# Optimization experiments

Hardware: AMD Instinct MI355X
Metric: run time of the kernel (lower is better)

## Reference

```python
import jax, jax.numpy as jnp
import numpy as np

N_POINTS = 1_500_000
N_SUPERPOINTS = 50_000
FEAT_DIM = 32
HIDDEN_DIM = 64
EMBED_DIM = 128


def setup_inputs() -> dict:
    key = jax.random.key(0)
    k1, k2, k3, k4, k5, k6 = jax.random.split(key, 6)
    return {
        "full_features": jax.random.normal(k1, (N_POINTS, FEAT_DIM), dtype=jnp.float32),
        "super_indices": jax.random.randint(k2, (N_POINTS,), 0, N_SUPERPOINTS, dtype=jnp.int64)
        if jax.config.jax_enable_x64 else jax.random.randint(k2, (N_POINTS,), 0, N_SUPERPOINTS, dtype=jnp.int32),
        "W1": jax.random.normal(k3, (FEAT_DIM, HIDDEN_DIM), dtype=jnp.float32) * 0.1,
        "b1": jax.random.normal(k4, (HIDDEN_DIM,), dtype=jnp.float32) * 0.01,
        "W2": jax.random.normal(k5, (HIDDEN_DIM, EMBED_DIM), dtype=jnp.float32) * 0.1,
        "b2": jax.random.normal(k6, (EMBED_DIM,), dtype=jnp.float32) * 0.01,
    }


def reference(full_features, super_indices, W1, b1, W2, b2):
    # Fused gather -> 2-layer MLP -> per-superpoint max reduction.
    # Equivalent to SuperPointNet.gen_token_embed, vectorized over all
    # superpoints instead of a Python loop with boolean-mask gathers.
    h = jax.nn.relu(full_features @ W1 + b1)          # [N, HIDDEN]
    h = jax.nn.relu(h @ W2 + b2)                      # [N, EMBED]
    sp_features = jax.ops.segment_max(
        h, super_indices, num_segments=N_SUPERPOINTS, indices_are_sorted=False
    )                                                  # [NS, EMBED]
    # Guard empty superpoints (segment_max yields -inf); original loop
    # assumes every superpoint id is present.
    sp_features = jnp.where(jnp.isfinite(sp_features), sp_features, 0.0)
    return sp_features
```

## Files before the change

kernel.cpp:

```cpp
#include <hip/hip_runtime.h>
#include <hip/hip_bf16.h>


#define NPTS 1500000
#define NSEG 50000
#define CAP  120

typedef __attribute__((ext_vector_type(8))) short short8;
typedef __attribute__((ext_vector_type(4))) float floatx4;
typedef __attribute__((ext_vector_type(2))) float floatx2;

__device__ __forceinline__ unsigned short f2bf(float f) {
    unsigned int x = __float_as_uint(f);
    x += 0x7FFFu + ((x >> 16) & 1u);
    return (unsigned short)(x >> 16);
}
__device__ __forceinline__ float bf2f(unsigned short b) {
    return __uint_as_float(((unsigned int)b) << 16);
}
__device__ __forceinline__ unsigned cvt_pk_bf16(float lo, float hi) {
    unsigned r;
    asm("v_cvt_pk_bf16_f32 %0, %1, %2" : "=v"(r) : "v"(lo), "v"(hi));
    return r;
}

__device__ __forceinline__ short8 load_x(const void* Xv, int pid, int quad, int isbf)
{
    if (isbf) {
        return *(const short8*)((const unsigned short*)Xv + (size_t)pid * 32 + quad * 8);
    } else {
        const float* xf = (const float*)Xv + (size_t)pid * 32 + quad * 8;
        const floatx4 f0 = *(const floatx4*)xf;
        const floatx4 f1 = *(const floatx4*)(xf + 4);
        union { short8 s; unsigned u[4]; } a;
        a.u[0] = cvt_pk_bf16(f0[0], f0[1]);
        a.u[1] = cvt_pk_bf16(f0[2], f0[3]);
        a.u[2] = cvt_pk_bf16(f1[0], f1[1]);
        a.u[3] = cvt_pk_bf16(f1[2], f1[3]);
        return a.s;
    }
}

__device__ __forceinline__ int probe_idx64(const unsigned* idxw, unsigned* scnt)
{
    if (threadIdx.x == 0) *scnt = 0u;
    __syncthreads();
    int nz = 0;
    #pragma unroll
    for (int j = 0; j < 2; ++j)
        nz += (idxw[(threadIdx.x * 2 + j) * 2 + 1] != 0u) ? 1 : 0;
    atomicAdd(scnt, (unsigned)nz);
    __syncthreads();
    return (*scnt < 256u) ? 1 : 0;
}

__device__ __forceinline__ int probe_isbf(const unsigned* Xw, unsigned* scnt)
{
    if (threadIdx.x == 0) *scnt = 0u;
    __syncthreads();
    int c = 0;
    #pragma unroll
    for (int j = 0; j < 4; ++j) {
        unsigned u  = Xw[threadIdx.x * 4 + j];
        unsigned he = (u >> 23) & 0xFFu, le = (u >> 7) & 0xFFu;
        c += (he >= 100u && he <= 140u && le >= 100u && le <= 140u) ? 1 : 0;
    }
    atomicAdd(scnt, (unsigned)c);
    __syncthreads();
    return (*scnt >= 512u) ? 1 : 0;
}

__global__ __launch_bounds__(256)
void build_slots(const unsigned* __restrict__ idxw,
                 const unsigned* __restrict__ Xw,
                 unsigned* __restrict__ cnt,
                 int* __restrict__ slots,
                 unsigned* __restrict__ flags)
{
    __shared__ unsigned sc;
    const int idx64 = probe_idx64(idxw, &sc);

    if (blockIdx.x == 0) {
        __syncthreads();
        const int isbf = probe_isbf(Xw, &sc);
        if (threadIdx.x == 0) flags[0] = (unsigned)isbf;
    }

    const int S  = gridDim.x * 256;
    const int i0 = blockIdx.x * 256 + threadIdx.x;
    const int i1 = i0 + S, i2 = i1 + S;

    unsigned s0 = 0xFFFFFFFFu, s1 = 0xFFFFFFFFu, s2 = 0xFFFFFFFFu;
    if (i0 < NPTS) s0 = idx64 ? idxw[2 * (size_t)i0] : idxw[i0];
    if (i1 < NPTS) s1 = idx64 ? idxw[2 * (size_t)i1] : idxw[i1];
    if (i2 < NPTS) s2 = idx64 ? idxw[2 * (size_t)i2] : idxw[i2];

    unsigned p0 = 0, p1 = 0, p2 = 0;
    if (s0 < NSEG) p0 = atomicAdd(&cnt[s0], 1u);
    if (s1 < NSEG) p1 = atomicAdd(&cnt[s1], 1u);
    if (s2 < NSEG) p2 = atomicAdd(&cnt[s2], 1u);

    if (s0 < NSEG && p0 < CAP) slots[(size_t)s0 * CAP + p0] = i0;
    if (s1 < NSEG && p1 < CAP) slots[(size_t)s1 * CAP + p1] = i1;
    if (s2 < NSEG && p2 < CAP) slots[(size_t)s2 * CAP + p2] = i2;
}

template<int DT>
__global__ __launch_bounds__(256)
void seg_mlp_max(const void* __restrict__ Xv,
                 const void* __restrict__ W1v, const void* __restrict__ B1v,
                 const void* __restrict__ W2v, const void* __restrict__ B2v,
                 const unsigned* __restrict__ cnt,
                 const int* __restrict__ slots,
                 const unsigned* __restrict__ flags,
                 void* __restrict__ outv)
{
    if (flags[0] != (unsigned)DT) return;

    __shared__ __align__(16) float outs[4][128];

    const int tid = threadIdx.x, wave = tid >> 6, lane = tid & 63;
    const int quad = lane >> 4, l16 = lane & 15;

    short8 w1f[4];
    #pragma unroll
    for (int t = 0; t < 4; ++t)
        #pragma unroll
        for (int j = 0; j < 8; ++j) {
            const int e = (quad * 8 + j) * 64 + t * 16 + l16;
            w1f[t][j] = DT ? (short)((const unsigned short*)W1v)[e]
                           : (short)f2bf(((const float*)W1v)[e]);
        }

    short8 w2f[2][8];
    #pragma unroll
    for (int kt = 0; kt < 2; ++kt)
        #pragma unroll
        for (int t = 0; t < 8; ++t)
            #pragma unroll
            for (int j = 0; j < 8; ++j) {
                const int k = kt * 32 + (j >> 2) * 16 + quad * 4 + (j & 3);
                const int e = k * 128 + t * 16 + l16;
                w2f[kt][t][j] = DT ? (short)((const unsigned short*)W2v)[e]
                                   : (short)f2bf(((const float*)W2v)[e]);
            }

    float b1v[16];
    #pragma unroll
    for (int t = 0; t < 4; ++t)
        #pragma unroll
        for (int r = 0; r < 4; ++r) {
            const int n = t * 16 + quad * 4 + r;
            b1v[t * 4 + r] = DT ? bf2f(((const unsigned short*)B1v)[n])
                                : ((const float*)B1v)[n];
        }
    float b2v[8];
    #pragma unroll
    for (int t = 0; t < 8; ++t)
        b2v[t] = DT ? bf2f(((const unsigned short*)B2v)[t * 16 + l16])
                    : ((const float*)B2v)[t * 16 + l16];

    float* fs = outs[wave];
    const int gw = blockIdx.x * 4 + wave, nw = gridDim.x * 4;

    for (int seg = gw; seg < NSEG; seg += nw) {
        const int c = min((int)cnt[seg], CAP);

        float vmax[8];
        #pragma unroll
        for (int t = 0; t < 8; ++t) vmax[t] = 0.f;

        if (c > 0) {
            const int nt = (c + 15) >> 4, last = c - 1;
            const size_t base = (size_t)seg * CAP;

            short8 abuf[2];
            abuf[0] = load_x(Xv, slots[base + min(l16, last)], quad, DT);
            if (nt > 1)
                abuf[1] = load_x(Xv, slots[base + min(16 + l16, last)], quad, DT);

            for (int ti = 0; ti < nt; ++ti) {
                const short8 acur = abuf[ti & 1];
                if (ti + 2 < nt)
                    abuf[ti & 1] = load_x(
                        Xv, slots[base + min((ti + 2) * 16 + l16, last)], quad, DT);

                floatx4 c1[4];
                #pragma unroll
                for (int t = 0; t < 4; ++t) {
                    floatx4 z = {0.f, 0.f, 0.f, 0.f};
                    c1[t] = __builtin_amdgcn_mfma_f32_16x16x32_bf16(w1f[t], acur, z, 0, 0, 0);
                }

                union { short8 s; unsigned u[4]; } af0, af1;
                #pragma unroll
                for (int t = 0; t < 4; ++t) {
                    const float h0 = fmaxf(c1[t][0] + b1v[t * 4 + 0], 0.f);
                    const float h1 = fmaxf(c1[t][1] + b1v[t * 4 + 1], 0.f);
                    const float h2 = fmaxf(c1[t][2] + b1v[t * 4 + 2], 0.f);
                    const float h3 = fmaxf(c1[t][3] + b1v[t * 4 + 3], 0.f);
                    const unsigned lo = cvt_pk_bf16(h0, h1);
                    const unsigned hi = cvt_pk_bf16(h2, h3);
                    if (t == 0)      { af0.u[0] = lo; af0.u[1] = hi; }
                    else if (t == 1) { af0.u[2] = lo; af0.u[3] = hi; }
                    else if (t == 2) { af1.u[0] = lo; af1.u[1] = hi; }
                    else             { af1.u[2] = lo; af1.u[3] = hi; }
                }

                #pragma unroll
                for (int t = 0; t < 8; ++t) {
                    floatx4 c4 = {0.f, 0.f, 0.f, 0.f};
                    c4 = __builtin_amdgcn_mfma_f32_16x16x32_bf16(af0.s, w2f[0][t], c4, 0, 0, 0);
                    c4 = __builtin_amdgcn_mfma_f32_16x16x32_bf16(af1.s, w2f[1][t], c4, 0, 0, 0);
                    #pragma unroll
                    for (int r = 0; r < 4; ++r)
                        vmax[t] = fmaxf(fmaxf(vmax[t], c4[r] + b2v[t]), 0.f);
                }
            }
        }

        #pragma unroll
        for (int t = 0; t < 8; ++t) {
            vmax[t] = fmaxf(vmax[t], __shfl_xor(vmax[t], 16, 64));
            vmax[t] = fmaxf(vmax[t], __shfl_xor(vmax[t], 32, 64));
        }
        if (quad == 0) {
            #pragma unroll
            for (int t = 0; t < 8; ++t) fs[t * 16 + l16] = vmax[t];
        }
        __builtin_amdgcn_s_waitcnt(0xC07F);
        const floatx2 o2 = ((const floatx2*)fs)[lane];
        if (DT) {
            ((unsigned*)outv)[seg * 64 + lane] = cvt_pk_bf16(o2[0], o2[1]);
        } else {
            ((floatx2*)outv)[seg * 64 + lane] = o2;
        }
        __builtin_amdgcn_s_waitcnt(0xC07F);
    }
}

extern "C" void kernel_launch(void* const* d_in, const int* in_sizes, int n_in,
                              void* d_out, int out_size, void* d_ws, size_t ws_size,
                              hipStream_t stream)
{
    const void* X   = d_in[0];
    const void* idx = d_in[1];
    const void* W1  = d_in[2];
    const void* B1  = d_in[3];
    const void* W2  = d_in[4];
    const void* B2  = d_in[5];

    char* w = (char*)d_ws;
    unsigned* cnt   = (unsigned*)w;  w += ((size_t)NSEG * 4 + 63) & ~63ull;
    unsigned* flags = (unsigned*)w;  w += 64;
    int*      slots = (int*)w;

    hipMemsetAsync(cnt, 0, (size_t)NSEG * 4, stream);
    build_slots<<<2048, 256, 0, stream>>>((const unsigned*)idx, (const unsigned*)X,
                                          cnt, slots, flags);
    seg_mlp_max<1><<<4096, 256, 0, stream>>>(X, W1, B1, W2, B2, cnt, slots, flags, d_out);
    seg_mlp_max<0><<<4096, 256, 0, stream>>>(X, W1, B1, W2, B2, cnt, slots, flags, d_out);
}
```

Measured before the change: 556.3 us.

## Scatter bf16 feature rows into per-segment contiguous buffers during bucketing

The bucketing kernel now also converts each point's features to bf16 and writes them into a dense per-superpoint row buffer (up to 64 rows). The MLP kernel then reads contiguous tiles instead of gathering by index, prefetches the next segment's count and tiles, and masks padded rows rather than clamping to duplicates. This removes the random gather in the compute kernel, at the cost of an extra write pass of about 200MB, a larger workspace requirement, and a fallback path for oversized segments.

```diff
diff --git a/kernel.cpp b/kernel.cpp
--- a/kernel.cpp
+++ b/kernel.cpp
@@ -5,10 +5,12 @@
 #define NPTS 1500000
 #define NSEG 50000
 #define CAP  120
+#define CAPX 64
 
 typedef __attribute__((ext_vector_type(8))) short short8;
 typedef __attribute__((ext_vector_type(4))) float floatx4;
 typedef __attribute__((ext_vector_type(2))) float floatx2;
+typedef __attribute__((ext_vector_type(4))) unsigned int uintx4;
 
 __device__ __forceinline__ unsigned short f2bf(float f) {
     unsigned int x = __float_as_uint(f);
@@ -43,6 +45,7 @@
 
 __device__ __forceinline__ int probe_idx64(const unsigned* idxw, unsigned* scnt)
 {
+    __syncthreads();
     if (threadIdx.x == 0) *scnt = 0u;
     __syncthreads();
     int nz = 0;
@@ -56,6 +59,7 @@
 
 __device__ __forceinline__ int probe_isbf(const unsigned* Xw, unsigned* scnt)
 {
+    __syncthreads();
     if (threadIdx.x == 0) *scnt = 0u;
     __syncthreads();
     int c = 0;
@@ -68,6 +72,255 @@
     atomicAdd(scnt, (unsigned)c);
     __syncthreads();
     return (*scnt >= 512u) ? 1 : 0;
+}
+
+__device__ __forceinline__ void load_row(const unsigned* Xw, int i, int isbf, uintx4 r[4])
+{
+    if (isbf) {
+        const uintx4* s = (const uintx4*)((const char*)Xw + (size_t)i * 64);
+        r[0] = s[0]; r[1] = s[1]; r[2] = s[2]; r[3] = s[3];
+    } else {
+        const floatx4* f = (const floatx4*)((const char*)Xw + (size_t)i * 128);
+        #pragma unroll
+        for (int k = 0; k < 4; ++k) {
+            const floatx4 a = f[2 * k], b = f[2 * k + 1];
+            uintx4 w;
+            w[0] = cvt_pk_bf16(a[0], a[1]);
+            w[1] = cvt_pk_bf16(a[2], a[3]);
+            w[2] = cvt_pk_bf16(b[0], b[1]);
+            w[3] = cvt_pk_bf16(b[2], b[3]);
+            r[k] = w;
+        }
+    }
+}
+
+__global__ __launch_bounds__(256)
+void build_rows(const unsigned* __restrict__ idxw,
+                const unsigned* __restrict__ Xw,
+                unsigned* __restrict__ cnt,
+                int* __restrict__ slots,
+                unsigned short* __restrict__ Xs,
+                unsigned* __restrict__ flags)
+{
+    __shared__ unsigned sc;
+    const int idx64 = probe_idx64(idxw, &sc);
+    const int isbf  = probe_isbf(Xw, &sc);
+    if (blockIdx.x == 0 && threadIdx.x == 0) flags[0] = (unsigned)isbf;
+
+    const int S  = gridDim.x * 256;
+    const int i0 = blockIdx.x * 256 + threadIdx.x;
+    const int i1 = i0 + S;
+
+    unsigned s0 = 0xFFFFFFFFu, s1 = 0xFFFFFFFFu;
+    if (i0 < NPTS) s0 = idx64 ? idxw[2 * (size_t)i0] : idxw[i0];
+    if (i1 < NPTS) s1 = idx64 ? idxw[2 * (size_t)i1] : idxw[i1];
+
+    uintx4 r0[4], r1[4];
+    if (s0 < NSEG) load_row(Xw, i0, isbf, r0);
+    if (s1 < NSEG) load_row(Xw, i1, isbf, r1);
+
+    unsigned p0 = 0, p1 = 0;
+    if (s0 < NSEG) p0 = atomicAdd(&cnt[s0], 1u);
+    if (s1 < NSEG) p1 = atomicAdd(&cnt[s1], 1u);
+
+    if (s0 < NSEG) {
+        if (p0 < CAP)  slots[(size_t)s0 * CAP + p0] = i0;
+        if (p0 < CAPX) {
+            uintx4* d = (uintx4*)(Xs + ((size_t)s0 * CAPX + p0) * 32);
+            d[0] = r0[0]; d[1] = r0[1]; d[2] = r0[2]; d[3] = r0[3];
+        }
+    }
+    if (s1 < NSEG) {
+        if (p1 < CAP)  slots[(size_t)s1 * CAP + p1] = i1;
+        if (p1 < CAPX) {
+            uintx4* d = (uintx4*)(Xs + ((size_t)s1 * CAPX + p1) * 32);
+            d[0] = r1[0]; d[1] = r1[1]; d[2] = r1[2]; d[3] = r1[3];
+        }
+    }
+}
+
+__device__ __forceinline__ void tile_mlp(const short8 acur,
+                                         const short8 w1f[4],
+                                         const short8 w2f[2][8],
+                                         const float b1v[16],
+                                         const float b2v[8],
+                                         float vmax[8],
+                                         const int quad,
+                                         const int lim, const bool full)
+{
+    floatx4 c1[4];
+    #pragma unroll
+    for (int t = 0; t < 4; ++t) {
+        floatx4 z = {0.f, 0.f, 0.f, 0.f};
+        c1[t] = __builtin_amdgcn_mfma_f32_16x16x32_bf16(w1f[t], acur, z, 0, 0, 0);
+    }
+
+    union { short8 s; unsigned u[4]; } af0, af1;
+    #pragma unroll
+    for (int t = 0; t < 4; ++t) {
+        const float h0 = fmaxf(c1[t][0] + b1v[t * 4 + 0], 0.f);
+        const float h1 = fmaxf(c1[t][1] + b1v[t * 4 + 1], 0.f);
+        const float h2 = fmaxf(c1[t][2] + b1v[t * 4 + 2], 0.f);
+        const float h3 = fmaxf(c1[t][3] + b1v[t * 4 + 3], 0.f);
+        const unsigned lo = cvt_pk_bf16(h0, h1);
+        const unsigned hi = cvt_pk_bf16(h2, h3);
+        if (t == 0)      { af0.u[0] = lo; af0.u[1] = hi; }
+        else if (t == 1) { af0.u[2] = lo; af0.u[3] = hi; }
+        else if (t == 2) { af1.u[0] = lo; af1.u[1] = hi; }
+        else             { af1.u[2] = lo; af1.u[3] = hi; }
+    }
+
+    #pragma unroll
+    for (int t = 0; t < 8; ++t) {
+        floatx4 c4 = {0.f, 0.f, 0.f, 0.f};
+        c4 = __builtin_amdgcn_mfma_f32_16x16x32_bf16(af0.s, w2f[0][t], c4, 0, 0, 0);
+        c4 = __builtin_amdgcn_mfma_f32_16x16x32_bf16(af1.s, w2f[1][t], c4, 0, 0, 0);
+        #pragma unroll
+        for (int r = 0; r < 4; ++r) {
+            const float v = c4[r] + b2v[t];
+            vmax[t] = fmaxf(vmax[t], (full || (quad * 4 + r) < lim) ? v : 0.f);
+        }
+    }
+}
+
+__device__ __forceinline__ short8 row_tile(const unsigned short* Xs, int seg,
+                                           int ti, int l16, int quad)
+{
+    return *(const short8*)(Xs + ((size_t)seg * CAPX + ti * 16 + l16) * 32 + quad * 8);
+}
+
+template<int DT>
+__global__ __launch_bounds__(256)
+void seg_mlp_rows(const void* __restrict__ Xv,
+                  const void* __restrict__ W1v, const void* __restrict__ B1v,
+                  const void* __restrict__ W2v, const void* __restrict__ B2v,
+                  const unsigned* __restrict__ cnt,
+                  const int* __restrict__ slots,
+                  const unsigned short* __restrict__ Xs,
+                  const unsigned* __restrict__ flags,
+                  void* __restrict__ outv)
+{
+    if (flags[0] != (unsigned)DT) return;
+
+    __shared__ __align__(16) float outs[4][128];
+
+    const int tid = threadIdx.x, wave = tid >> 6, lane = tid & 63;
+    const int quad = lane >> 4, l16 = lane & 15;
+
+    short8 w1f[4];
+    #pragma unroll
+    for (int t = 0; t < 4; ++t)
+        #pragma unroll
+        for (int j = 0; j < 8; ++j) {
+            const int e = (quad * 8 + j) * 64 + t * 16 + l16;
+            w1f[t][j] = DT ? (short)((const unsigned short*)W1v)[e]
+                           : (short)f2bf(((const float*)W1v)[e]);
+        }
+
+    short8 w2f[2][8];
+    #pragma unroll
+    for (int kt = 0; kt < 2; ++kt)
+        #pragma unroll
+        for (int t = 0; t < 8; ++t)
+            #pragma unroll
+            for (int j = 0; j < 8; ++j) {
+                const int k = kt * 32 + (j >> 2) * 16 + quad * 4 + (j & 3);
+                const int e = k * 128 + t * 16 + l16;
+                w2f[kt][t][j] = DT ? (short)((const unsigned short*)W2v)[e]
+                                   : (short)f2bf(((const float*)W2v)[e]);
+            }
+
+    float b1v[16];
+    #pragma unroll
+    for (int t = 0; t < 4; ++t)
+        #pragma unroll
+        for (int r = 0; r < 4; ++r) {
+            const int n = t * 16 + quad * 4 + r;
+            b1v[t * 4 + r] = DT ? bf2f(((const unsigned short*)B1v)[n])
+                                : ((const float*)B1v)[n];
+        }
+    float b2v[8];
+    #pragma unroll
+    for (int t = 0; t < 8; ++t)
+        b2v[t] = DT ? bf2f(((const unsigned short*)B2v)[t * 16 + l16])
+                    : ((const float*)B2v)[t * 16 + l16];
+
+    float* fs = outs[wave];
+    const int gw = blockIdx.x * 4 + wave, nw = gridDim.x * 4;
+
+    unsigned c_cur = 0;
+    short8 r0 = {}, r1 = {};
+    if (gw < NSEG) {
+        c_cur = cnt[gw];
+        r0 = row_tile(Xs, gw, 0, l16, quad);
+        r1 = row_tile(Xs, gw, 1, l16, quad);
+    }
+
+    for (int seg = gw; seg < NSEG; seg += nw) {
+        const int c_raw = (int)c_cur;
+        const int c  = min(c_raw, CAPX);
+        const int nt = (c + 15) >> 4;
+
+        short8 r2 = {}, r3 = {};
+        if (nt > 2) r2 = row_tile(Xs, seg, 2, l16, quad);
+        if (nt > 3) r3 = row_tile(Xs, seg, 3, l16, quad);
+
+        const int segn = seg + nw;
+        unsigned cn = 0;
+        short8 r0n = {}, r1n = {};
+        if (segn < NSEG) {
+            cn  = cnt[segn];
+            r0n = row_tile(Xs, segn, 0, l16, quad);
+            r1n = row_tile(Xs, segn, 1, l16, quad);
+        }
+
+        float vmax[8];
+        #pragma unroll
+        for (int t = 0; t < 8; ++t) vmax[t] = 0.f;
+
+        if (c_raw > CAPX) {
+            const int c2 = min(c_raw, CAP);
+            const int nt2 = (c2 + 15) >> 4, last = c2 - 1;
+            const size_t base = (size_t)seg * CAP;
+            for (int ti = 0; ti < nt2; ++ti) {
+                int pid = slots[base + min(ti * 16 + l16, last)];
+                pid = min(max(pid, 0), NPTS - 1);
+                const short8 acur = load_x(Xv, pid, quad, DT);
+                tile_mlp(acur, w1f, w2f, b1v, b2v, vmax, quad, 16, true);
+            }
+        } else if (c > 0) {
+            #pragma unroll
+            for (int ti = 0; ti < 4; ++ti) {
+                if (ti < nt) {
+                    const short8 acur = (ti == 0) ? r0 : (ti == 1) ? r1
+                                      : (ti == 2) ? r2 : r3;
+                    const int lim = c - ti * 16;
+                    tile_mlp(acur, w1f, w2f, b1v, b2v, vmax, quad,
+                             lim, lim >= 16);
+                }
+            }
+        }
+
+        #pragma unroll
+        for (int t = 0; t < 8; ++t) {
+            vmax[t] = fmaxf(vmax[t], __shfl_xor(vmax[t], 16, 64));
+            vmax[t] = fmaxf(vmax[t], __shfl_xor(vmax[t], 32, 64));
+        }
+        if (quad == 0) {
+            #pragma unroll
+            for (int t = 0; t < 8; ++t) fs[t * 16 + l16] = vmax[t];
+        }
+        __builtin_amdgcn_s_waitcnt(0xC07F);
+        const floatx2 o2 = ((const floatx2*)fs)[lane];
+        if (DT) {
+            ((unsigned*)outv)[seg * 64 + lane] = cvt_pk_bf16(o2[0], o2[1]);
+        } else {
+            ((floatx2*)outv)[seg * 64 + lane] = o2;
+        }
+        __builtin_amdgcn_s_waitcnt(0xC07F);
+
+        c_cur = cn; r0 = r0n; r1 = r1n;
+    }
 }
 
 __global__ __launch_bounds__(256)
@@ -81,7 +334,6 @@
     const int idx64 = probe_idx64(idxw, &sc);
 
     if (blockIdx.x == 0) {
-        __syncthreads();
         const int isbf = probe_isbf(Xw, &sc);
         if (threadIdx.x == 0) flags[0] = (unsigned)isbf;
     }
@@ -131,7 +383,6 @@
             w1f[t][j] = DT ? (short)((const unsigned short*)W1v)[e]
                            : (short)f2bf(((const float*)W1v)[e]);
         }
-
     short8 w2f[2][8];
     #pragma unroll
     for (int kt = 0; kt < 2; ++kt)
@@ -144,7 +395,6 @@
                 w2f[kt][t][j] = DT ? (short)((const unsigned short*)W2v)[e]
                                    : (short)f2bf(((const float*)W2v)[e]);
             }
-
     float b1v[16];
     #pragma unroll
     for (int t = 0; t < 4; ++t)
@@ -184,38 +434,7 @@
                 if (ti + 2 < nt)
                     abuf[ti & 1] = load_x(
                         Xv, slots[base + min((ti + 2) * 16 + l16, last)], quad, DT);
-
-                floatx4 c1[4];
-                #pragma unroll
-                for (int t = 0; t < 4; ++t) {
-                    floatx4 z = {0.f, 0.f, 0.f, 0.f};
-                    c1[t] = __builtin_amdgcn_mfma_f32_16x16x32_bf16(w1f[t], acur, z, 0, 0, 0);
-                }
-
-                union { short8 s; unsigned u[4]; } af0, af1;
-                #pragma unroll
-                for (int t = 0; t < 4; ++t) {
-                    const float h0 = fmaxf(c1[t][0] + b1v[t * 4 + 0], 0.f);
-                    const float h1 = fmaxf(c1[t][1] + b1v[t * 4 + 1], 0.f);
-                    const float h2 = fmaxf(c1[t][2] + b1v[t * 4 + 2], 0.f);
-                    const float h3 = fmaxf(c1[t][3] + b1v[t * 4 + 3], 0.f);
-                    const unsigned lo = cvt_pk_bf16(h0, h1);
-                    const unsigned hi = cvt_pk_bf16(h2, h3);
-                    if (t == 0)      { af0.u[0] = lo; af0.u[1] = hi; }
-                    else if (t == 1) { af0.u[2] = lo; af0.u[3] = hi; }
-                    else if (t == 2) { af1.u[0] = lo; af1.u[1] = hi; }
-                    else             { af1.u[2] = lo; af1.u[3] = hi; }
-                }
-
-                #pragma unroll
-                for (int t = 0; t < 8; ++t) {
-                    floatx4 c4 = {0.f, 0.f, 0.f, 0.f};
-                    c4 = __builtin_amdgcn_mfma_f32_16x16x32_bf16(af0.s, w2f[0][t], c4, 0, 0, 0);
-                    c4 = __builtin_amdgcn_mfma_f32_16x16x32_bf16(af1.s, w2f[1][t], c4, 0, 0, 0);
-                    #pragma unroll
-                    for (int r = 0; r < 4; ++r)
-                        vmax[t] = fmaxf(fmaxf(vmax[t], c4[r] + b2v[t]), 0.f);
-                }
+                tile_mlp(acur, w1f, w2f, b1v, b2v, vmax, quad, 16, true);
             }
         }
 
@@ -253,11 +472,28 @@
     char* w = (char*)d_ws;
     unsigned* cnt   = (unsigned*)w;  w += ((size_t)NSEG * 4 + 63) & ~63ull;
     unsigned* flags = (unsigned*)w;  w += 64;
-    int*      slots = (int*)w;
+    int*      slots = (int*)w;       w += (size_t)NSEG * CAP * 4;
+    unsigned short* Xs = (unsigned short*)w;
+
+    const size_t need_fast =
+        (((size_t)NSEG * 4 + 63) & ~63ull) + 64 +
+        (size_t)NSEG * CAP * 4 + (size_t)NSEG * CAPX * 64;
 
     hipMemsetAsync(cnt, 0, (size_t)NSEG * 4, stream);
-    build_slots<<<2048, 256, 0, stream>>>((const unsigned*)idx, (const unsigned*)X,
-                                          cnt, slots, flags);
-    seg_mlp_max<1><<<4096, 256, 0, stream>>>(X, W1, B1, W2, B2, cnt, slots, flags, d_out);
-    seg_mlp_max<0><<<4096, 256, 0, stream>>>(X, W1, B1, W2, B2, cnt, slots, flags, d_out);
-}
+
+    if (ws_size >= need_fast) {
+        build_rows<<<3072, 256, 0, stream>>>((const unsigned*)idx, (const unsigned*)X,
+                                             cnt, slots, Xs, flags);
+        seg_mlp_rows<1><<<4096, 256, 0, stream>>>(X, W1, B1, W2, B2, cnt, slots,
+                                                  Xs, flags, d_out);
+        seg_mlp_rows<0><<<4096, 256, 0, stream>>>(X, W1, B1, W2, B2, cnt, slots,
+                                                  Xs, flags, d_out);
+    } else {
+        build_slots<<<2048, 256, 0, stream>>>((const unsigned*)idx, (const unsigned*)X,
+                                              cnt, slots, flags);
+        seg_mlp_max<1><<<4096, 256, 0, stream>>>(X, W1, B1, W2, B2, cnt, slots,
+                                                 flags, d_out);
+        seg_mlp_max<0><<<4096, 256, 0, stream>>>(X, W1, B1, W2, B2, cnt, slots,
+                                                 flags, d_out);
+    }
+}
```

After: 449.3 us. 1.24x faster.
